# Performance work log

Measured on AMD Instinct MI355X. Metric: run time of the kernel, lower is better.

Reference implementation:

```python
import jax, jax.numpy as jnp
import numpy as np

HEADS = 8
DIM_HEAD = 64
SCALE = DIM_HEAD ** (-0.5)
EPS = 1e-5


def setup_inputs() -> dict:
    key = jax.random.key(0)
    k1, k2, k3, k4 = jax.random.split(key, 4)
    b, c, t = 16, 512, 4096
    hidden = HEADS * DIM_HEAD
    x = jax.random.normal(k1, (b, c, t), dtype=jnp.float32)
    W_qkv = jax.random.normal(k2, (hidden * 3, c), dtype=jnp.float32) * (c ** -0.5)
    W_out = jax.random.normal(k3, (c, hidden), dtype=jnp.float32) * (hidden ** -0.5)
    b_out = jax.random.normal(k4, (c,), dtype=jnp.float32) * 0.02
    gn_w = jnp.ones((c,), dtype=jnp.float32)
    gn_b = jnp.zeros((c,), dtype=jnp.float32)
    return {"x": x, "W_qkv": W_qkv, "W_out": W_out, "b_out": b_out,
            "gn_w": gn_w, "gn_b": gn_b}


def reference(x, W_qkv, W_out, b_out, gn_w, gn_b):
    b, c, t = x.shape
    # 1x1 conv = channel matmul: [3*hidden, c] @ [b, c, t] -> [b, 3*hidden, t]
    qkv = jnp.einsum('oc,bct->bot', W_qkv, x)
    q, k, v = jnp.split(qkv, 3, axis=1)
    q = q.reshape(b, HEADS, DIM_HEAD, t)
    k = k.reshape(b, HEADS, DIM_HEAD, t)
    v = v.reshape(b, HEADS, DIM_HEAD, t)
    q = jax.nn.softmax(q, axis=-2) * SCALE  # softmax over feature dim
    k = jax.nn.softmax(k, axis=-1)          # softmax over time dim
    # context = k @ v^T : [b,h,dk,t] x [b,h,t,dv] -> [b,h,dk,dv]
    context = jnp.einsum('bhdt,bhet->bhde', k, v)
    # out = context^T @ q : [b,h,dv,dk] x [b,h,dk,t] -> [b,h,dv,t]
    out = jnp.einsum('bhde,bhdt->bhet', context, q)
    out = out.reshape(b, HEADS * DIM_HEAD, t)
    # output 1x1 conv with bias
    out = jnp.einsum('oc,bct->bot', W_out, out) + b_out[None, :, None]
    # GroupNorm(1, dim): normalize over (channels, time) per sample
    mean = jnp.mean(out, axis=(1, 2), keepdims=True)
    var = jnp.var(out, axis=(1, 2), keepdims=True)
    out = (out - mean) * jax.lax.rsqrt(var + EPS)
    out = out * gn_w[None, :, None] + gn_b[None, :, None]
    return out
```

## Files before the change

kernel.cpp:

```cpp
#include <hip/hip_runtime.h>
#include <stdint.h>

#define B_ 16
#define C_ 512
#define T_ 4096
#define H_ 8
#define D_ 64
#define SCALE_ 0.125f
#define EPS_ 1e-5f

using ushortT = unsigned short;
using ushort8 = __attribute__((ext_vector_type(8))) unsigned short;
using short8  = __attribute__((ext_vector_type(8))) short;
using floatx4 = __attribute__((ext_vector_type(4))) float;

__device__ __forceinline__ float bf2f(ushortT u) {
  union { unsigned int i; float f; } x; x.i = ((unsigned int)u) << 16; return x.f;
}
__device__ __forceinline__ ushortT f2bf(float f) {
  union { float f; unsigned int i; } x; x.f = f;
  unsigned int r = x.i + 0x7fffu + ((x.i >> 16) & 1u);
  return (ushortT)(r >> 16);
}

#define GLD16(gp, lp)                                                          \
  __builtin_amdgcn_global_load_lds(                                            \
      (const __attribute__((address_space(1))) unsigned int*)(gp),             \
      (__attribute__((address_space(3))) unsigned int*)(lp), 16, 0, 0)

__global__ __launch_bounds__(256) void cvt_f32_bf16(const float* __restrict__ src,
                                                    ushortT* __restrict__ dst, int n4) {
  int i = blockIdx.x * 256 + threadIdx.x;
  if (i >= n4) return;
  floatx4 v = *(const floatx4*)(src + (size_t)i * 4);
  unsigned int p0 = (unsigned int)f2bf(v[0]) | ((unsigned int)f2bf(v[1]) << 16);
  unsigned int p1 = (unsigned int)f2bf(v[2]) | ((unsigned int)f2bf(v[3]) << 16);
  *(unsigned long long*)(dst + (size_t)i * 4) =
      (unsigned long long)p0 | ((unsigned long long)p1 << 32);
}

__global__ void zero_f32(float* p, int n4) {
  int i = blockIdx.x * 256 + threadIdx.x;
  if (i < n4) ((floatx4*)p)[i] = (floatx4){0.f, 0.f, 0.f, 0.f};
}

__global__ __launch_bounds__(256) void transpose_x(const float* __restrict__ x,
                                                   ushortT* __restrict__ xT) {
  __shared__ ushortT tile[64][65];
  int b = blockIdx.z;
  int t0 = blockIdx.x * 64, c0 = blockIdx.y * 64;
  const float* xb = x + (size_t)b * C_ * T_;
  ushortT* xTb = xT + (size_t)b * T_ * C_;
  for (int i = threadIdx.x; i < 4096; i += 256) {
    int cc = i >> 6, tt = i & 63;
    tile[cc][tt] = f2bf(xb[(size_t)(c0 + cc) * T_ + t0 + tt]);
  }
  __syncthreads();
  for (int i = threadIdx.x; i < 4096; i += 256) {
    int tt = i >> 6, cc = i & 63;
    xTb[(size_t)(t0 + tt) * C_ + c0 + cc] = tile[cc][tt];
  }
}

template <int MODE>
__global__ __launch_bounds__(256) void gemm_bt(
    const ushortT* __restrict__ A, const ushortT* __restrict__ Bt,
    void* __restrict__ Cc, const float* __restrict__ bias,
    float* __restrict__ stats,
    int K, int lda, int ldb, int ldc,
    unsigned long long bsA, unsigned long long bsB, unsigned long long bsC) {
  __shared__ ushortT As[128 * 64];
  __shared__ ushortT Bs[128 * 64];
  unsigned int gx = gridDim.x, gy = gridDim.y;
  unsigned int nwg = gx * gy * gridDim.z;
  unsigned int lin = blockIdx.x + gx * (blockIdx.y + gy * blockIdx.z);
  unsigned int cpx = nwg >> 3;
  unsigned int wid = (lin & 7u) * cpx + (lin >> 3);
  unsigned int bx = wid % gx;
  unsigned int tmp = wid / gx;
  unsigned int by = tmp % gy;
  unsigned int bz = tmp / gy;

  const int b = bz;
  A += (size_t)b * bsA; Bt += (size_t)b * bsB;
  const int m0 = by * 128, n0 = bx * 128;
  const int tid = threadIdx.x;
  const int w = tid >> 6, l = tid & 63;
  const int wm = (w >> 1) * 64, wn = (w & 1) * 64;
  const int quad = l >> 4, ln = l & 15;
  floatx4 acc[4][4];
#pragma unroll
  for (int i = 0; i < 4; i++)
#pragma unroll
    for (int j = 0; j < 4; j++) acc[i][j] = (floatx4){0.f, 0.f, 0.f, 0.f};

  for (int kb = 0; kb < K; kb += 64) {
#pragma unroll
    for (int i = 0; i < 4; ++i) {
      int wci = i * 256 + (tid & 192);
      int ci  = wci + (tid & 63);
      int row = ci >> 3;
      int scol = ((ci & 7) ^ (row & 7)) << 3;
      GLD16(&A[(size_t)(m0 + row) * lda + kb + scol], &As[wci * 8]);
      GLD16(&Bt[(size_t)(n0 + row) * ldb + kb + scol], &Bs[wci * 8]);
    }
    __syncthreads();
#pragma unroll
    for (int kk = 0; kk < 2; ++kk) {
      short8 af[4], bfv[4];
#pragma unroll
      for (int i = 0; i < 4; i++)
        af[i] = *(const short8*)(
            &As[(wm + i * 16 + ln) * 64 + (((kk * 4 + quad) ^ (ln & 7)) << 3)]);
#pragma unroll
      for (int j = 0; j < 4; j++)
        bfv[j] = *(const short8*)(
            &Bs[(wn + j * 16 + ln) * 64 + (((kk * 4 + quad) ^ (ln & 7)) << 3)]);
#pragma unroll
      for (int i = 0; i < 4; i++)
#pragma unroll
        for (int j = 0; j < 4; j++)
          acc[i][j] = __builtin_amdgcn_mfma_f32_16x16x32_bf16(af[i], bfv[j], acc[i][j], 0, 0, 0);
    }
    __syncthreads();
  }

  if constexpr (MODE == 4) {
    const bool isk = (m0 < 512);
    ushortT* Co = (ushortT*)Cc + (size_t)b * bsC;
#pragma unroll
    for (int i = 0; i < 4; i++)
#pragma unroll
      for (int r = 0; r < 4; r++) {
        int row = m0 + wm + i * 16 + quad * 4 + r;
#pragma unroll
        for (int j = 0; j < 4; j++) {
          int col = n0 + wn + j * 16 + ln;
          float v = acc[i][j][r];
          if (isk) v = expf(v);
          Co[(size_t)row * ldc + col] = f2bf(v);
        }
      }
  } else if constexpr (MODE == 2) {
    ushortT* Co = (ushortT*)Cc + (size_t)b * bsC;
#pragma unroll
    for (int i = 0; i < 4; i++)
#pragma unroll
      for (int r = 0; r < 4; r++) {
        float v0 = acc[i][0][r], v1 = acc[i][1][r], v2 = acc[i][2][r], v3 = acc[i][3][r];
        float mx = fmaxf(fmaxf(v0, v1), fmaxf(v2, v3));
#pragma unroll
        for (int off = 1; off < 16; off <<= 1) mx = fmaxf(mx, __shfl_xor(mx, off));
        float e0 = expf(v0 - mx), e1 = expf(v1 - mx);
        float e2 = expf(v2 - mx), e3 = expf(v3 - mx);
        float s = (e0 + e1) + (e2 + e3);
#pragma unroll
        for (int off = 1; off < 16; off <<= 1) s += __shfl_xor(s, off);
        float inv = SCALE_ / s;
        int row = m0 + wm + i * 16 + quad * 4 + r;
        size_t base = (size_t)row * ldc + n0 + wn + ln;
        Co[base +  0] = f2bf(e0 * inv);
        Co[base + 16] = f2bf(e1 * inv);
        Co[base + 32] = f2bf(e2 * inv);
        Co[base + 48] = f2bf(e3 * inv);
      }
  } else {
    float* Co = (float*)Cc + (size_t)b * bsC;
    float s = 0.f, ss = 0.f;
#pragma unroll
    for (int i = 0; i < 4; i++)
#pragma unroll
      for (int r = 0; r < 4; r++) {
        int row = m0 + wm + i * 16 + quad * 4 + r;
        float bv = bias ? bias[row] : 0.f;
#pragma unroll
        for (int j = 0; j < 4; j++) {
          int col = n0 + wn + j * 16 + ln;
          float v = acc[i][j][r] + bv;
          Co[(size_t)row * ldc + col] = v;
          s += v; ss += v * v;
        }
      }
#pragma unroll
    for (int off = 1; off < 64; off <<= 1) {
      s += __shfl_xor(s, off);
      ss += __shfl_xor(ss, off);
    }
    __shared__ float rs[4], rss[4];
    if (l == 0) { rs[w] = s; rss[w] = ss; }
    __syncthreads();
    if (tid == 0) {
      atomicAdd(&stats[b * 2],     rs[0] + rs[1] + rs[2] + rs[3]);
      atomicAdd(&stats[b * 2 + 1], rss[0] + rss[1] + rss[2] + rss[3]);
    }
  }
}

__global__ __launch_bounds__(64) void context_kv(const ushortT* __restrict__ kv,
                                                 float* __restrict__ ksum,
                                                 float* __restrict__ ct) {
  __shared__ ushortT Vs[64 * 32];
  __shared__ ushortT Ks[64 * 32];
  const int slice = blockIdx.x, h = blockIdx.y, b = blockIdx.z;
  const int t0 = slice * 256;
  const ushortT* vrow = kv + ((size_t)b * 1024 + 512 + h * 64) * T_;
  const ushortT* krow = kv + ((size_t)b * 1024 + h * 64) * T_;
  const int tid = threadIdx.x, quad = tid >> 4, ln = tid & 15;
  float rsum[4] = {0.f, 0.f, 0.f, 0.f};
  floatx4 acc[4][4];
#pragma unroll
  for (int i = 0; i < 4; i++)
#pragma unroll
    for (int j = 0; j < 4; j++) acc[i][j] = (floatx4){0.f, 0.f, 0.f, 0.f};
  for (int kb = 0; kb < 256; kb += 32) {
#pragma unroll
    for (int i = 0; i < 4; ++i) {
      int ci = i * 64 + tid;
      int row = ci >> 2, col = (ci & 3) << 3;
      GLD16(&vrow[(size_t)row * T_ + t0 + kb + col], &Vs[i * 512]);
      GLD16(&krow[(size_t)row * T_ + t0 + kb + col], &Ks[i * 512]);
    }
    __syncthreads();
    short8 af[4], bfv[4];
#pragma unroll
    for (int i = 0; i < 4; i++) af[i] = *(const short8*)(&Vs[(i * 16 + ln) * 32 + quad * 8]);
#pragma unroll
    for (int j = 0; j < 4; j++) {
      bfv[j] = *(const short8*)(&Ks[(j * 16 + ln) * 32 + quad * 8]);
#pragma unroll
      for (int e = 0; e < 8; e++) rsum[j] += bf2f((ushortT)bfv[j][e]);
    }
#pragma unroll
    for (int i = 0; i < 4; i++)
#pragma unroll
      for (int j = 0; j < 4; j++)
        acc[i][j] = __builtin_amdgcn_mfma_f32_16x16x32_bf16(af[i], bfv[j], acc[i][j], 0, 0, 0);
    __syncthreads();
  }
  float* ks = ksum + (size_t)b * 512 + h * 64;
#pragma unroll
  for (int j = 0; j < 4; ++j) {
    float s = rsum[j];
    s += __shfl_xor(s, 16);
    s += __shfl_xor(s, 32);
    if (quad == 0) atomicAdd(&ks[j * 16 + ln], s);
  }
  float* ctbh = ct + (size_t)(b * 8 + h) * 4096;
#pragma unroll
  for (int i = 0; i < 4; i++)
#pragma unroll
    for (int r = 0; r < 4; r++) {
      int e = i * 16 + quad * 4 + r;
#pragma unroll
      for (int j = 0; j < 4; j++) {
        int d = j * 16 + ln;
        atomicAdd(&ctbh[e * 64 + d], acc[i][j][r]);
      }
    }
}

__global__ __launch_bounds__(64) void ct_combine(const ushortT* __restrict__ Wobf,
                                                 const float* __restrict__ ct,
                                                 const float* __restrict__ ksum,
                                                 ushortT* __restrict__ W2) {
  __shared__ ushortT As[64 * 64];
  __shared__ float Cs[64 * 64];
  const int c0 = blockIdx.x * 64, h = blockIdx.y, b = blockIdx.z;
  const int tid = threadIdx.x, quad = tid >> 4, ln = tid & 15;
  const float* ctbh = ct + (size_t)(b * 8 + h) * 4096;
#pragma unroll
  for (int i = 0; i < 8; ++i) {
    int ci = i * 64 + tid;
    int row = ci >> 3, col = (ci & 7) << 3;
    *(uint4*)(&As[row * 64 + col]) = *(const uint4*)(&Wobf[(size_t)(c0 + row) * 512 + h * 64 + col]);
  }
#pragma unroll
  for (int i = 0; i < 16; ++i) {
    int off = (i * 64 + tid) * 4;
    *(floatx4*)(&Cs[off]) = *(const floatx4*)(&ctbh[off]);
  }
  const float* ks = ksum + (size_t)b * 512 + h * 64;
  float invd[4];
#pragma unroll
  for (int j = 0; j < 4; j++) invd[j] = 1.f / ks[j * 16 + ln];
  __syncthreads();
  floatx4 acc[4][4];
#pragma unroll
  for (int i = 0; i < 4; i++)
#pragma unroll
    for (int j = 0; j < 4; j++) acc[i][j] = (floatx4){0.f, 0.f, 0.f, 0.f};
#pragma unroll
  for (int kk = 0; kk < 2; ++kk) {
    short8 af[4], bfv[4];
#pragma unroll
    for (int i = 0; i < 4; i++) af[i] = *(const short8*)(&As[(i * 16 + ln) * 64 + kk * 32 + quad * 8]);
#pragma unroll
    for (int j = 0; j < 4; j++) {
#pragma unroll
      for (int e2 = 0; e2 < 8; ++e2)
        bfv[j][e2] = (short)f2bf(Cs[(kk * 32 + quad * 8 + e2) * 64 + j * 16 + ln] * invd[j]);
    }
#pragma unroll
    for (int i = 0; i < 4; i++)
#pragma unroll
      for (int j = 0; j < 4; j++)
        acc[i][j] = __builtin_amdgcn_mfma_f32_16x16x32_bf16(af[i], bfv[j], acc[i][j], 0, 0, 0);
  }
  ushortT* W2b = W2 + (size_t)b * 512 * 512;
#pragma unroll
  for (int i = 0; i < 4; i++)
#pragma unroll
    for (int r = 0; r < 4; r++) {
      int row = c0 + i * 16 + quad * 4 + r;
#pragma unroll
      for (int j = 0; j < 4; j++) {
        int col = h * 64 + j * 16 + ln;
        W2b[(size_t)row * 512 + col] = f2bf(acc[i][j][r]);
      }
    }
}

__global__ __launch_bounds__(256) void gn_apply(float* __restrict__ out,
                                                const float* __restrict__ stats,
                                                const float* __restrict__ gnw,
                                                const float* __restrict__ gnb) {
  int b = blockIdx.y;
  int i = blockIdx.x * 256 + threadIdx.x;
  const float invN = 1.f / (float)(C_ * T_);
  float mean = stats[b * 2] * invN;
  float var = stats[b * 2 + 1] * invN - mean * mean;
  float inv = rsqrtf(var + EPS_);
  int c = i >> 9;
  float wv = gnw[c] * inv, bv = gnb[c];
  float* p = out + (size_t)b * C_ * T_ + (size_t)i * 8;
  floatx4 v0 = *(const floatx4*)p;
  floatx4 v1 = *(const floatx4*)(p + 4);
#pragma unroll
  for (int j = 0; j < 4; j++) v0[j] = (v0[j] - mean) * wv + bv;
#pragma unroll
  for (int j = 0; j < 4; j++) v1[j] = (v1[j] - mean) * wv + bv;
  *(floatx4*)p = v0;
  *(floatx4*)(p + 4) = v1;
}

extern "C" void kernel_launch(void* const* d_in, const int* in_sizes, int n_in,
                              void* d_out, int out_size, void* d_ws, size_t ws_size,
                              hipStream_t stream) {
  (void)in_sizes; (void)n_in; (void)out_size; (void)ws_size;
  const float* x    = (const float*)d_in[0];
  const float* Wqkv = (const float*)d_in[1];
  const float* Wout = (const float*)d_in[2];
  const float* bout = (const float*)d_in[3];
  const float* gnw  = (const float*)d_in[4];
  const float* gnb  = (const float*)d_in[5];
  float* out = (float*)d_out;

  char* ws = (char*)d_ws;
  ushortT* xT   = (ushortT*)(ws);
  ushortT* qT   = (ushortT*)(ws + 67108864);
  ushortT* Wqbf = (ushortT*)(ws + 134217728);
  ushortT* Wobf = (ushortT*)(ws + 135790592);
  float*   ct   = (float*)(ws + 136314880);
  float* stats  = (float*)(ws + 138412032);
  float* ksum   = (float*)(ws);
  ushortT* W2   = (ushortT*)(ws + 1048576);
  ushortT* kv   = (ushortT*)d_out;

  cvt_f32_bf16<<<768, 256, 0, stream>>>(Wqkv, Wqbf, 196608);
  cvt_f32_bf16<<<256, 256, 0, stream>>>(Wout, Wobf, 65536);
  zero_f32<<<513, 256, 0, stream>>>(ct, 131080);

  transpose_x<<<dim3(64, 8, 16), 256, 0, stream>>>(x, xT);

  gemm_bt<4><<<dim3(32, 8, 16), 256, 0, stream>>>(
      Wqbf + 512 * 512, xT, kv, nullptr, nullptr, 512, 512, 512, 4096,
      0ULL, (unsigned long long)(T_ * 512), (unsigned long long)(1024 * T_));

  gemm_bt<2><<<dim3(4, 32, 16), 256, 0, stream>>>(
      xT, Wqbf, qT, nullptr, nullptr, 512, 512, 512, 512,
      (unsigned long long)(T_ * 512), 0ULL, (unsigned long long)(T_ * 512));

  zero_f32<<<8, 256, 0, stream>>>(ksum, 2048);

  context_kv<<<dim3(16, 8, 16), 64, 0, stream>>>(kv, ksum, ct);

  ct_combine<<<dim3(8, 8, 16), 64, 0, stream>>>(Wobf, ct, ksum, W2);

  gemm_bt<3><<<dim3(32, 4, 16), 256, 0, stream>>>(
      W2, qT, out, bout, stats, 512, 512, 512, 4096,
      (unsigned long long)(512 * 512), (unsigned long long)(T_ * 512),
      (unsigned long long)(512 * T_));

  gn_apply<<<dim3(1024, 16), 256, 0, stream>>>(out, stats, gnw, gnb);
}
```

Before: 567.4 us.

## Double-buffer GEMM shared-memory tiles to overlap global loads with MFMA

The bf16 GEMM kernel now keeps two LDS buffers for A and B and issues the direct-to-LDS loads for the next K tile before computing on the current one. Explicit vmcnt waits let the current tile's loads finish while the next tile's eight loads stay in flight. The aim is to hide global memory latency behind the MFMA work. In exchange, LDS use doubles to 64KB per block, which may lower occupancy, and the hand-written waitcnt and barrier sequence is fragile.

```diff
diff --git a/kernel.cpp b/kernel.cpp
--- a/kernel.cpp
+++ b/kernel.cpp
@@ -62,6 +62,19 @@
   }
 }
 
+#define STAGE_TILE(KB, BUF)                                                    \
+  {                                                                            \
+    _Pragma("unroll")                                                          \
+    for (int i_ = 0; i_ < 4; ++i_) {                                           \
+      int wci_ = i_ * 256 + (tid & 192);                                       \
+      int ci_  = wci_ + (tid & 63);                                            \
+      int row_ = ci_ >> 3;                                                     \
+      int scol_ = ((ci_ & 7) ^ (row_ & 7)) << 3;                               \
+      GLD16(&A[(size_t)(m0 + row_) * lda + (KB) + scol_], &As[BUF][wci_ * 8]); \
+      GLD16(&Bt[(size_t)(n0 + row_) * ldb + (KB) + scol_], &Bs[BUF][wci_ * 8]);\
+    }                                                                          \
+  }
+
 template <int MODE>
 __global__ __launch_bounds__(256) void gemm_bt(
     const ushortT* __restrict__ A, const ushortT* __restrict__ Bt,
@@ -69,8 +82,8 @@
     float* __restrict__ stats,
     int K, int lda, int ldb, int ldc,
     unsigned long long bsA, unsigned long long bsB, unsigned long long bsC) {
-  __shared__ ushortT As[128 * 64];
-  __shared__ ushortT Bs[128 * 64];
+  __shared__ ushortT As[2][128 * 64];
+  __shared__ ushortT Bs[2][128 * 64];
   unsigned int gx = gridDim.x, gy = gridDim.y;
   unsigned int nwg = gx * gy * gridDim.z;
   unsigned int lin = blockIdx.x + gx * (blockIdx.y + gy * blockIdx.z);
@@ -94,35 +107,38 @@
 #pragma unroll
     for (int j = 0; j < 4; j++) acc[i][j] = (floatx4){0.f, 0.f, 0.f, 0.f};
 
-  for (int kb = 0; kb < K; kb += 64) {
-#pragma unroll
-    for (int i = 0; i < 4; ++i) {
-      int wci = i * 256 + (tid & 192);
-      int ci  = wci + (tid & 63);
-      int row = ci >> 3;
-      int scol = ((ci & 7) ^ (row & 7)) << 3;
-      GLD16(&A[(size_t)(m0 + row) * lda + kb + scol], &As[wci * 8]);
-      GLD16(&Bt[(size_t)(n0 + row) * ldb + kb + scol], &Bs[wci * 8]);
-    }
-    __syncthreads();
+  STAGE_TILE(0, 0);
+  const int nt = K >> 6;
+  for (int t = 0; t < nt; ++t) {
+    const int cur = t & 1;
+    if (t + 1 < nt) {
+      STAGE_TILE((t + 1) << 6, cur ^ 1);
+      asm volatile("s_waitcnt vmcnt(8)" ::: "memory");
+    } else {
+      asm volatile("s_waitcnt vmcnt(0)" ::: "memory");
+    }
+    __builtin_amdgcn_s_barrier();
+    asm volatile("" ::: "memory");
 #pragma unroll
     for (int kk = 0; kk < 2; ++kk) {
       short8 af[4], bfv[4];
 #pragma unroll
       for (int i = 0; i < 4; i++)
         af[i] = *(const short8*)(
-            &As[(wm + i * 16 + ln) * 64 + (((kk * 4 + quad) ^ (ln & 7)) << 3)]);
+            &As[cur][(wm + i * 16 + ln) * 64 + (((kk * 4 + quad) ^ (ln & 7)) << 3)]);
 #pragma unroll
       for (int j = 0; j < 4; j++)
         bfv[j] = *(const short8*)(
-            &Bs[(wn + j * 16 + ln) * 64 + (((kk * 4 + quad) ^ (ln & 7)) << 3)]);
+            &Bs[cur][(wn + j * 16 + ln) * 64 + (((kk * 4 + quad) ^ (ln & 7)) << 3)]);
 #pragma unroll
       for (int i = 0; i < 4; i++)
 #pragma unroll
         for (int j = 0; j < 4; j++)
           acc[i][j] = __builtin_amdgcn_mfma_f32_16x16x32_bf16(af[i], bfv[j], acc[i][j], 0, 0, 0);
     }
-    __syncthreads();
+    asm volatile("s_waitcnt lgkmcnt(0)" ::: "memory");
+    __builtin_amdgcn_s_barrier();
+    asm volatile("" ::: "memory");
   }
 
   if constexpr (MODE == 4) {
```

After: 589.8 us. 1.04x slower.
